# Kernel optimization log

Hardware: AMD Instinct MI355X
Metric: run time of the kernel (lower is better)

## Reference

```python
import jax, jax.numpy as jnp
import numpy as np

N = 8192
HID = 256
LAMBDA = 1.0
MU = 1.0
DIM = 2
GC = 0.0027
L = 0.02
Y0, Y1 = 0.0, 1.0
STRESS_PRE_SCALE = 1.0
PF_PRE_SCALE = 1.0


def loading(t):
    # linear displacement loading
    return t[0]


def mlp(Ws, bs, inp):
    h = inp
    for W, b in zip(Ws[:-1], bs[:-1]):
        h = jnp.tanh(h @ W + b)
    return h @ Ws[-1] + bs[-1]


def net_u(Ws, bs, x, t):
    sol = mlp(Ws, bs, jnp.concatenate([x, t]))  # (3,)
    phi = jax.nn.sigmoid(sol[:1])               # (1,)
    ld = loading(t)
    ux = (x[1] - Y0) * (x[1] - Y1) * sol[1:2] * ld / 3.0
    uy = (x[1] - Y0) * (x[1] - Y1) * sol[2:3] * ld + (x[1] - Y0) / (Y1 - Y0) * ld
    return phi, jnp.concatenate([ux, uy])       # (1,), (2,)


def epsilon_fn(Ws, bs, x, t):
    J = jax.jacrev(lambda xx: net_u(Ws, bs, xx, t)[1])(x)  # (2,2)
    return (J + J.T) / 2.0


def psi_pos(eps):
    tr = jnp.trace(eps)
    k = LAMBDA + MU * 2.0 / DIM
    dev = eps - tr * jnp.eye(DIM, dtype=eps.dtype) / DIM
    return k * jax.nn.relu(tr) ** 2 / 2 + MU * jnp.trace(dev @ dev)


def psi_neg(eps):
    k = LAMBDA + MU * 2.0 / DIM
    return k * jax.nn.relu(-jnp.trace(eps)) ** 2 / 2


def sigma_fn(Ws, bs, x, t):
    phi, _ = net_u(Ws, bs, x, t)
    g_phi = (1 - phi[0]) ** 2 + 1e-6
    eps = epsilon_fn(Ws, bs, x, t)
    return g_phi * jax.grad(psi_pos)(eps) + jax.grad(psi_neg)(eps)


def net_stress(Ws, bs, x, t):
    def damaged(xx):
        phi, _ = net_u(Ws, bs, xx, t)
        return (1 - phi) ** 2 * sigma_fn(Ws, bs, xx, t)  # (2,2)
    D = jax.jacrev(damaged)(x)          # (2,2,2)
    return jnp.einsum('ijj->i', D) / STRESS_PRE_SCALE


def net_pf_raw(Ws, bs, x, t):
    phi, _ = net_u(Ws, bs, x, t)
    phi0 = phi[0]
    eps = epsilon_fn(Ws, bs, x, t)
    H = jax.hessian(lambda xx: net_u(Ws, bs, xx, t)[0])(x)[0]  # (2,2)
    lap_phi = jnp.trace(H)
    pf = GC * (phi0 / L - L * lap_phi) - 2 * (1 - phi0) * psi_pos(eps)
    return pf / PF_PRE_SCALE


def net_speed(Ws, bs, x, t):
    return jax.jacrev(lambda tt: net_u(Ws, bs, x, tt)[0])(t)[0, 0]


def net_pf(Ws, bs, x, t):
    pf = net_pf_raw(Ws, bs, x, t)
    dphi_dt = net_speed(Ws, bs, x, t)
    phi0 = net_u(Ws, bs, x, t)[0][0]
    mask_pos = (jnp.abs(dphi_dt) <= 1e-3) & (jnp.abs(phi0 - 1) > 1e-3)
    mask_neg = jnp.abs(phi0 - 1) <= 1e-3
    return jnp.where(mask_pos, jax.nn.relu(-pf), jnp.where(mask_neg, jax.nn.relu(pf), pf))


def net_energy(Ws, bs, x, t):
    phi0 = net_u(Ws, bs, x, t)[0][0]
    eps = epsilon_fn(Ws, bs, x, t)
    nphi = jax.jacrev(lambda xx: net_u(Ws, bs, xx, t)[0])(x)[0]  # (2,)
    return ((1 - phi0) * 2 * psi_pos(eps) + psi_neg(eps)
            + GC * (phi0 ** 2 / (2 * L) + L / 2 * jnp.sum(nphi ** 2)))


def _forward(W0, W1, W2, W3, W4, b0, b1, b2, b3, b4, x, t):
    Ws = [W0, W1, W2, W3, W4]
    bs = [b0, b1, b2, b3, b4]
    res_s = jax.vmap(net_stress, in_axes=(None, None, 0, 0))(Ws, bs, x, t)   # (N,2)
    res_pf = jax.vmap(net_pf, in_axes=(None, None, 0, 0))(Ws, bs, x, t)     # (N,)
    res_e = jax.vmap(net_energy, in_axes=(None, None, 0, 0))(Ws, bs, x, t)  # (N,)
    dphi = jax.vmap(net_speed, in_axes=(None, None, 0, 0))(Ws, bs, x, t)    # (N,)
    # component re-weighting for the vector stress residual (as in loss_pde)
    mse_res = jnp.mean(res_s ** 2, axis=0)  # (2,)
    w = jax.lax.stop_gradient(jnp.mean(mse_res) / (mse_res + 1e-6))
    r = jnp.sqrt(jnp.sum(res_s ** 2 * w[None, :], axis=-1))
    loss_stress = jnp.mean(r ** 2)
    loss_pf = jnp.mean(res_pf ** 2)
    loss_energy = jnp.log(jnp.sum(res_e))
    loss_irr = jnp.mean(jax.nn.relu(-dphi))
    return jnp.stack([loss_stress, loss_pf, loss_energy, loss_irr])


def setup_inputs() -> dict:
    key = jax.random.key(0)
    dims = [3, HID, HID, HID, HID, 3]
    ks = jax.random.split(key, 12)
    inp = {}
    for i in range(5):
        fan_in, fan_out = dims[i], dims[i + 1]
        inp[f'W{i}'] = (jax.random.normal(ks[i], (fan_in, fan_out), jnp.float32)
                        * np.sqrt(2.0 / (fan_in + fan_out)).astype(np.float32))
        inp[f'b{i}'] = jnp.zeros((fan_out,), jnp.float32)
    inp['x'] = jax.random.uniform(ks[10], (N, 2), jnp.float32, 0.0, 1.0)
    inp['t'] = jax.random.uniform(ks[11], (N, 1), jnp.float32, 0.05, 1.0)
    return inp


def reference(W0, W1, W2, W3, W4, b0, b1, b2, b3, b4, x, t):
    return _forward(W0, W1, W2, W3, W4, b0, b1, b2, b3, b4, x, t)
```

## Files before the change

### kernel.cpp

```cpp
#include <hip/hip_runtime.h>
#include <math.h>

#define N_PTS 8192
#define HIDDEN 256
#define PPB 8
#define THREADS 256
#define NBLK (N_PTS / PPB)
#define NBINS 64
#define LDA 264
#define AROWS 62
#define LDZ 264
#define BP_OFF 4096

typedef float f32x4 __attribute__((ext_vector_type(4)));
typedef short s8v  __attribute__((ext_vector_type(8)));
typedef short s4v  __attribute__((ext_vector_type(4)));

__device__ __forceinline__ unsigned short bf16_rne(float x) {
    unsigned int u = __float_as_uint(x);
    return (unsigned short)((u + 0x7FFFu + ((u >> 16) & 1u)) >> 16);
}
__device__ __forceinline__ float bf16f(unsigned short h) {
    return __uint_as_float(((unsigned int)h) << 16);
}
__device__ __forceinline__ int rowof(int s, int p) {
    return (s < 6) ? ((s >> 1) * 16 + (p >> 1) * 4 + (p & 1) * 2 + (s & 1))
                   : (48 + (p >> 1) * 4 + (p & 1));
}

__global__ void pinn_pack(const float* __restrict__ W1, const float* __restrict__ W2,
                          const float* __restrict__ W3, unsigned short* __restrict__ Bp,
                          float* __restrict__ bins)
{
    if (blockIdx.x == 0) {
        bins[threadIdx.x] = 0.f;
        bins[threadIdx.x + 256] = 0.f;
        if (threadIdx.x == 0) *(unsigned*)(bins + 512) = 0u;
    }
    const int id = blockIdx.x * 256 + threadIdx.x;
    const int lane = id & 63;
    const int nt   = (id >> 6) & 15;
    const int kc   = (id >> 10) & 7;
    const int l    = id >> 13;
    const float* W = (l == 0) ? W1 : ((l == 1) ? W2 : W3);
    const int n  = nt * 16 + (lane & 15);
    unsigned short hi[8], lo[8];
    #pragma unroll
    for (int i = 0; i < 8; ++i) {
        const int kslot = kc * 32 + (lane >> 4) * 8 + i;
        const int korig = ((kslot >> 6) & 3) * 64 + (kslot & 3) * 16 + ((kslot >> 2) & 15);
        const float x = W[(size_t)korig * HIDDEN + n];
        const unsigned short h = bf16_rne(x);
        hi[i] = h;
        lo[i] = bf16_rne(x - bf16f(h));
    }
    const size_t bh = ((((size_t)(l * 2 + 0) * 8 + kc) * 16 + nt) * 64 + lane) * 8;
    const size_t bl = ((((size_t)(l * 2 + 1) * 8 + kc) * 16 + nt) * 64 + lane) * 8;
    *(s8v*)&Bp[bh] = *(const s8v*)hi;
    *(s8v*)&Bp[bl] = *(const s8v*)lo;
}

__global__ __launch_bounds__(THREADS, 2)
void pinn_main(const float* __restrict__ W0, const float* __restrict__ b0,
               const float* __restrict__ b1, const float* __restrict__ b2,
               const float* __restrict__ b3,
               const float* __restrict__ W4, const float* __restrict__ b4,
               const float* __restrict__ xin, const float* __restrict__ tin,
               const unsigned short* __restrict__ Bp,
               float* __restrict__ bins, float* __restrict__ out)
{
    __shared__ __align__(16) unsigned char LB[65472];
    short* __restrict__ AhS = (short*)LB;
    short* __restrict__ AlS = (short*)(LB + AROWS * LDA * 2);
    float* __restrict__ Zf  = (float*)LB;

    const int tid  = threadIdx.x;
    const int lane = tid & 63;
    const int w    = tid >> 6;
    const int c    = lane & 15;
    const int g    = lane >> 4;
    const int pt0  = blockIdx.x * PPB;
    unsigned* cnt  = (unsigned*)(bins + 512);

    {
        const int c0i = tid & 15, w0i = (tid >> 4) & 3, pp = tid >> 6;
        float w0v[4], w1v[4], w2v[4], bbv[4];
        #pragma unroll
        for (int nn = 0; nn < 4; ++nn) {
            const int j = w0i * 64 + 16 * nn + c0i;
            w0v[nn] = W0[j]; w1v[nn] = W0[HIDDEN + j]; w2v[nn] = W0[2 * HIDDEN + j];
            bbv[nn] = b0[j];
        }
        const int sbase = 4 * (c0i + 16 * w0i);
        #pragma unroll
        for (int e = 0; e < 2; ++e) {
            const int p = pp + 4 * e;
            const float x0 = xin[(pt0 + p) * 2 + 0];
            const float x1 = xin[(pt0 + p) * 2 + 1];
            const float tt = tin[pt0 + p];
            s4v hi[7], lo[7];
            #pragma unroll
            for (int nn = 0; nn < 4; ++nn) {
                const float z  = fmaf(x0, w0v[nn], fmaf(x1, w1v[nn], fmaf(tt, w2v[nn], bbv[nn])));
                const float a  = tanhf(z);
                const float st = 1.f - a * a;
                const float m2 = -2.f * a * st;
                float v[7];
                v[0] = a;
                v[1] = st * w0v[nn]; v[2] = st * w1v[nn]; v[3] = st * w2v[nn];
                v[4] = m2 * w0v[nn] * w0v[nn];
                v[5] = m2 * w0v[nn] * w1v[nn];
                v[6] = m2 * w1v[nn] * w1v[nn];
                #pragma unroll
                for (int s = 0; s < 7; ++s) {
                    const unsigned short h = bf16_rne(v[s]);
                    hi[s][nn] = (short)h;
                    lo[s][nn] = (short)bf16_rne(v[s] - bf16f(h));
                }
            }
            #pragma unroll
            for (int s = 0; s < 7; ++s) {
                const int r = rowof(s, p);
                *(s4v*)&AhS[r * LDA + sbase] = hi[s];
                *(s4v*)&AlS[r * LDA + sbase] = lo[s];
            }
        }
        if (pp == 0) {
            const s4v z4 = {0, 0, 0, 0};
            #pragma unroll
            for (int b = 0; b < 3; ++b)
                #pragma unroll
                for (int d = 2; d < 4; ++d) {
                    const int r = 48 + 4 * b + d;
                    *(s4v*)&AhS[r * LDA + sbase] = z4;
                    *(s4v*)&AlS[r * LDA + sbase] = z4;
                }
        }
    }
    __syncthreads();

    int aoff[4];
    #pragma unroll
    for (int mt = 0; mt < 3; ++mt) aoff[mt] = (16 * mt + c) * LDA + g * 8;
    aoff[3] = (48 + ((c >= 14) ? 0 : c)) * LDA + g * 8;

    for (int l = 0; l < 3; ++l) {
        f32x4 acc[4][4];
        #pragma unroll
        for (int mt = 0; mt < 4; ++mt)
            #pragma unroll
            for (int nn = 0; nn < 4; ++nn) acc[mt][nn] = (f32x4)0.f;

        const size_t lbase = (size_t)l * 2 * 8 * 16 * 64 * 8;
        #pragma unroll
        for (int kc = 0; kc < 8; ++kc) {
            s8v ah[4], al[4];
            #pragma unroll
            for (int mt = 0; mt < 4; ++mt) {
                ah[mt] = *(const s8v*)&AhS[aoff[mt] + kc * 32];
                al[mt] = *(const s8v*)&AlS[aoff[mt] + kc * 32];
            }
            s8v bh[4], bl[4];
            #pragma unroll
            for (int nn = 0; nn < 4; ++nn) {
                const int nt = w * 4 + nn;
                const size_t oh = lbase + (((size_t)kc * 16 + nt) * 64 + lane) * 8;
                const size_t ol = oh + (size_t)8 * 16 * 64 * 8;
                bh[nn] = *(const s8v*)&Bp[oh];
                bl[nn] = *(const s8v*)&Bp[ol];
            }
            #pragma unroll
            for (int mt = 0; mt < 4; ++mt)
                #pragma unroll
                for (int nn = 0; nn < 4; ++nn) {
                    acc[mt][nn] = __builtin_amdgcn_mfma_f32_16x16x32_bf16(ah[mt], bh[nn], acc[mt][nn], 0, 0, 0);
                    acc[mt][nn] = __builtin_amdgcn_mfma_f32_16x16x32_bf16(ah[mt], bl[nn], acc[mt][nn], 0, 0, 0);
                    acc[mt][nn] = __builtin_amdgcn_mfma_f32_16x16x32_bf16(al[mt], bh[nn], acc[mt][nn], 0, 0, 0);
                }
        }
        __syncthreads();

        const float* bias = (l == 0) ? b1 : (l == 1) ? b2 : b3;
        float bbv[4];
        #pragma unroll
        for (int nn = 0; nn < 4; ++nn) bbv[nn] = bias[64 * w + 16 * nn + c];
        const int sbase = 4 * (c + 16 * w);

        #pragma unroll
        for (int e = 0; e < 2; ++e) {
            const int p = 2 * g + e;
            float v[7][4];
            #pragma unroll
            for (int nn = 0; nn < 4; ++nn) {
                const float z0 = acc[0][nn][2 * e + 0] + bbv[nn];
                const float z1 = acc[0][nn][2 * e + 1];
                const float z2 = acc[1][nn][2 * e + 0];
                const float z3 = acc[1][nn][2 * e + 1];
                const float z4 = acc[2][nn][2 * e + 0];
                const float z5 = acc[2][nn][2 * e + 1];
                const float z6 = acc[3][nn][e];
                const float a  = tanhf(z0);
                const float st = 1.f - a * a;
                const float m2 = -2.f * a * st;
                v[0][nn] = a;
                v[1][nn] = st * z1; v[2][nn] = st * z2; v[3][nn] = st * z3;
                v[4][nn] = fmaf(m2 * z1, z1, st * z4);
                v[5][nn] = fmaf(m2 * z1, z2, st * z5);
                v[6][nn] = fmaf(m2 * z2, z2, st * z6);
            }
            if (l < 2) {
                #pragma unroll
                for (int s = 0; s < 7; ++s) {
                    s4v hi, lo;
                    #pragma unroll
                    for (int nn = 0; nn < 4; ++nn) {
                        const unsigned short h = bf16_rne(v[s][nn]);
                        hi[nn] = (short)h;
                        lo[nn] = (short)bf16_rne(v[s][nn] - bf16f(h));
                    }
                    const int r = rowof(s, p);
                    *(s4v*)&AhS[r * LDA + sbase] = hi;
                    *(s4v*)&AlS[r * LDA + sbase] = lo;
                }
            } else {
                #pragma unroll
                for (int s = 0; s < 7; ++s) {
                    f32x4 vv = {v[s][0], v[s][1], v[s][2], v[s][3]};
                    *(f32x4*)&Zf[(8 * s + p) * LDZ + sbase] = vv;
                }
            }
        }
        __syncthreads();
    }

    const int h  = (lane >> 5);
    const int la = lane & 31;
    const int p  = w * 2 + h;

    float part[7][3];
    #pragma unroll
    for (int s = 0; s < 7; ++s)
        #pragma unroll
        for (int m = 0; m < 3; ++m) part[s][m] = 0.f;

    #pragma unroll
    for (int i = 0; i < 8; ++i) {
        const int kslot = la + 32 * i;
        const int korig = ((kslot >> 6) & 3) * 64 + (kslot & 3) * 16 + ((kslot >> 2) & 15);
        const float w40 = W4[korig * 3 + 0], w41 = W4[korig * 3 + 1], w42 = W4[korig * 3 + 2];
        #pragma unroll
        for (int s = 0; s < 7; ++s) {
            const float hk = Zf[(8 * s + p) * LDZ + kslot];
            part[s][0] = fmaf(hk, w40, part[s][0]);
            part[s][1] = fmaf(hk, w41, part[s][1]);
            part[s][2] = fmaf(hk, w42, part[s][2]);
        }
    }
    #pragma unroll
    for (int s = 0; s < 7; ++s)
        #pragma unroll
        for (int m = 0; m < 3; ++m) {
            float v = part[s][m];
            #pragma unroll
            for (int off = 16; off > 0; off >>= 1) v += __shfl_xor(v, off);
            part[s][m] = v;
        }

    const float x0 = xin[(pt0 + p) * 2 + 0];
    const float x1 = xin[(pt0 + p) * 2 + 1];
    const float tt = tin[pt0 + p];

    const float V0 = part[0][0] + b4[0];
    const float V1 = part[0][1] + b4[1];
    const float V2 = part[0][2] + b4[2];
    const float J00 = part[1][0], J01 = part[2][0], J0t = part[3][0];
    const float J10 = part[1][1], J11 = part[2][1];
    const float J20 = part[1][2], J21 = part[2][2];
    const float H000 = part[4][0], H011 = part[6][0];
    const float H100 = part[4][1], H101 = part[5][1], H111 = part[6][1];
    const float H200 = part[4][2], H201 = part[5][2], H211 = part[6][2];

    const float phi = 1.f / (1.f + expf(-V0));
    const float om  = 1.f - phi;
    const float sp  = phi * om;
    const float spp = sp * (1.f - 2.f * phi);
    const float phx0 = sp * J00, phx1 = sp * J01, dphidt = sp * J0t;
    const float lap = spp * (J00 * J00 + J01 * J01) + sp * (H000 + H011);

    const float ld = tt;
    const float qq = x1 * (x1 - 1.f), qp = 2.f * x1 - 1.f;

    const float ux0 = qq * J10 * ld * (1.f / 3.f);
    const float ux1 = (qp * V1 + qq * J11) * ld * (1.f / 3.f);
    const float uy0 = qq * J20 * ld;
    const float uy1 = (qp * V2 + qq * J21) * ld + ld;

    const float e00 = ux0, e11 = uy1, e01 = 0.5f * (ux1 + uy0);
    const float tr = e00 + e11;

    const float ux_00 = qq * H100 * ld * (1.f / 3.f);
    const float ux_01 = (qp * J10 + qq * H101) * ld * (1.f / 3.f);
    const float ux_11 = (2.f * V1 + 2.f * qp * J11 + qq * H111) * ld * (1.f / 3.f);
    const float uy_00 = qq * H200 * ld;
    const float uy_01 = (qp * J20 + qq * H201) * ld;
    const float uy_11 = (2.f * V2 + 2.f * qp * J21 + qq * H211) * ld;

    const float de00_0 = ux_00, de00_1 = ux_01;
    const float de11_0 = uy_01, de11_1 = uy_11;
    const float de01_0 = 0.5f * (ux_01 + uy_00), de01_1 = 0.5f * (ux_11 + uy_01);
    const float dtr_0 = de00_0 + de11_0, dtr_1 = de00_1 + de11_1;

    const float kk = 2.f;
    const float rtr = fmaxf(tr, 0.f), rntr = fmaxf(-tr, 0.f);
    const float Hp = (tr > 0.f) ? 1.f : 0.f, Hn = (tr < 0.f) ? 1.f : 0.f;

    const float dv = 0.5f * (e00 - e11);
    const float sp00 = kk * rtr + 2.f * dv;
    const float sp11 = kk * rtr - 2.f * dv;
    const float sp01 = 2.f * e01;
    const float snd  = -kk * rntr;

    const float dsp00_0 = kk * Hp * dtr_0 + 2.f * (de00_0 - 0.5f * dtr_0);
    const float dsp01_0 = 2.f * de01_0;
    const float dsp01_1 = 2.f * de01_1;
    const float dsp11_1 = kk * Hp * dtr_1 + 2.f * (de11_1 - 0.5f * dtr_1);
    const float dsn_0 = kk * Hn * dtr_0, dsn_1 = kk * Hn * dtr_1;

    const float cc  = om * om, gg = cc + 1e-6f;
    const float dc0 = -2.f * om * phx0, dc1 = -2.f * om * phx1;
    const float gpc = gg + cc, cg = cc * gg;

    const float res0 = dc0 * gpc * sp00 + cg * dsp00_0 + dc0 * snd + cc * dsn_0
                     + dc1 * gpc * sp01 + cg * dsp01_1;
    const float res1 = dc0 * gpc * sp01 + cg * dsp01_0
                     + dc1 * gpc * sp11 + cg * dsp11_1 + dc1 * snd + cc * dsn_1;

    const float psip = rtr * rtr + 0.5f * (e00 - e11) * (e00 - e11) + 2.f * e01 * e01;
    const float psin = rntr * rntr;

    const float GCc = 0.0027f, LL = 0.02f;
    const float pf = GCc * (phi / LL - LL * lap) - 2.f * om * psip;
    const bool maskp = (fabsf(dphidt) <= 1e-3f) && (fabsf(phi - 1.f) > 1e-3f);
    const bool maskn = fabsf(phi - 1.f) <= 1e-3f;
    const float respf = maskp ? fmaxf(-pf, 0.f) : (maskn ? fmaxf(pf, 0.f) : pf);

    const float rese = om * 2.f * psip + psin
                     + GCc * (phi * phi / (2.f * LL)
                              + 0.5f * LL * (phx0 * phx0 + phx1 * phx1));
    const float irr = fmaxf(-dphidt, 0.f);

    if (la == 0) {
        float* bin = bins + (blockIdx.x & (NBINS - 1)) * 8;
        atomicAdd(bin + 0, res0 * res0);
        atomicAdd(bin + 1, res1 * res1);
        atomicAdd(bin + 2, respf * respf);
        atomicAdd(bin + 3, rese);
        atomicAdd(bin + 4, irr);
    }

    __syncthreads();
    volatile unsigned* flg = (volatile unsigned*)(LB + 65024);
    if (tid == 0) {
        const unsigned old = atomicAdd(cnt, 1u);
        *flg = old;
    }
    __syncthreads();
    if (*flg == NBLK - 1) {
        if (tid < 64) {
            float s0 = atomicAdd(&bins[tid * 8 + 0], 0.f);
            float s1 = atomicAdd(&bins[tid * 8 + 1], 0.f);
            float s2 = atomicAdd(&bins[tid * 8 + 2], 0.f);
            float s3 = atomicAdd(&bins[tid * 8 + 3], 0.f);
            float s4 = atomicAdd(&bins[tid * 8 + 4], 0.f);
            #pragma unroll
            for (int off = 32; off > 0; off >>= 1) {
                s0 += __shfl_xor(s0, off);
                s1 += __shfl_xor(s1, off);
                s2 += __shfl_xor(s2, off);
                s3 += __shfl_xor(s3, off);
                s4 += __shfl_xor(s4, off);
            }
            if (tid == 0) {
                const float inv_n = 1.f / (float)N_PTS;
                const float mse0 = s0 * inv_n, mse1 = s1 * inv_n;
                const float wm = 0.5f * (mse0 + mse1);
                out[0] = wm * mse0 / (mse0 + 1e-6f) + wm * mse1 / (mse1 + 1e-6f);
                out[1] = s2 * inv_n;
                out[2] = logf(s3);
                out[3] = s4 * inv_n;
            }
        }
    }
}

extern "C" void kernel_launch(void* const* d_in, const int* in_sizes, int n_in,
                              void* d_out, int out_size, void* d_ws, size_t ws_size,
                              hipStream_t stream)
{
    const float *W[5], *b[5];
    if (in_sizes[1] == HIDDEN) {
        for (int i = 0; i < 5; ++i) {
            W[i] = (const float*)d_in[2 * i];
            b[i] = (const float*)d_in[2 * i + 1];
        }
    } else {
        for (int i = 0; i < 5; ++i) {
            W[i] = (const float*)d_in[i];
            b[i] = (const float*)d_in[5 + i];
        }
    }
    const float* x = (const float*)d_in[10];
    const float* t = (const float*)d_in[11];
    float* bins = (float*)d_ws;
    unsigned short* Bp = (unsigned short*)((char*)d_ws + BP_OFF);

    pinn_pack<<<96, 256, 0, stream>>>(W[1], W[2], W[3], Bp, bins);
    pinn_main<<<NBLK, THREADS, 0, stream>>>(W[0], b[0], b[1], b[2], b[3],
                                            W[4], b[4], x, t, Bp, bins,
                                            (float*)d_out);
}
```

Before: 155.1 us.

## Halve points per block and repack A rows to remove MFMA padding waste

```diff
diff --git a/kernel.cpp b/kernel.cpp
--- a/kernel.cpp
+++ b/kernel.cpp
@@ -3,12 +3,12 @@
 
 #define N_PTS 8192
 #define HIDDEN 256
-#define PPB 8
+#define PPB 4
 #define THREADS 256
 #define NBLK (N_PTS / PPB)
 #define NBINS 64
 #define LDA 264
-#define AROWS 62
+#define AROWS 32
 #define LDZ 264
 #define BP_OFF 4096
 
@@ -24,20 +24,15 @@
     return __uint_as_float(((unsigned int)h) << 16);
 }
 __device__ __forceinline__ int rowof(int s, int p) {
-    return (s < 6) ? ((s >> 1) * 16 + (p >> 1) * 4 + (p & 1) * 2 + (s & 1))
-                   : (48 + (p >> 1) * 4 + (p & 1));
+    return (s < 4) ? (4 * p + s) : (16 + 4 * p + (s - 4));
 }
 
 __global__ void pinn_pack(const float* __restrict__ W1, const float* __restrict__ W2,
                           const float* __restrict__ W3, unsigned short* __restrict__ Bp,
                           float* __restrict__ bins)
 {
-    if (blockIdx.x == 0) {
-        bins[threadIdx.x] = 0.f;
-        bins[threadIdx.x + 256] = 0.f;
-        if (threadIdx.x == 0) *(unsigned*)(bins + 512) = 0u;
-    }
-    const int id = blockIdx.x * 256 + threadIdx.x;
+    const int id = blockIdx.x * 64 + threadIdx.x;
+    if (id < 520) bins[id] = 0.f;
     const int lane = id & 63;
     const int nt   = (id >> 6) & 15;
     const int kc   = (id >> 10) & 7;
@@ -60,7 +55,7 @@
     *(s8v*)&Bp[bl] = *(const s8v*)lo;
 }
 
-__global__ __launch_bounds__(THREADS, 2)
+__global__ __launch_bounds__(THREADS, 4)
 void pinn_main(const float* __restrict__ W0, const float* __restrict__ b0,
                const float* __restrict__ b1, const float* __restrict__ b2,
                const float* __restrict__ b3,
@@ -69,7 +64,8 @@
                const unsigned short* __restrict__ Bp,
                float* __restrict__ bins, float* __restrict__ out)
 {
-    __shared__ __align__(16) unsigned char LB[65472];
+    __shared__ __align__(16) unsigned char LB[AROWS * LDA * 4];
+    __shared__ unsigned flagS;
     short* __restrict__ AhS = (short*)LB;
     short* __restrict__ AlS = (short*)(LB + AROWS * LDA * 2);
     float* __restrict__ Zf  = (float*)LB;
@@ -92,71 +88,59 @@
             bbv[nn] = b0[j];
         }
         const int sbase = 4 * (c0i + 16 * w0i);
-        #pragma unroll
-        for (int e = 0; e < 2; ++e) {
-            const int p = pp + 4 * e;
-            const float x0 = xin[(pt0 + p) * 2 + 0];
-            const float x1 = xin[(pt0 + p) * 2 + 1];
-            const float tt = tin[pt0 + p];
-            s4v hi[7], lo[7];
-            #pragma unroll
-            for (int nn = 0; nn < 4; ++nn) {
-                const float z  = fmaf(x0, w0v[nn], fmaf(x1, w1v[nn], fmaf(tt, w2v[nn], bbv[nn])));
-                const float a  = tanhf(z);
-                const float st = 1.f - a * a;
-                const float m2 = -2.f * a * st;
-                float v[7];
-                v[0] = a;
-                v[1] = st * w0v[nn]; v[2] = st * w1v[nn]; v[3] = st * w2v[nn];
-                v[4] = m2 * w0v[nn] * w0v[nn];
-                v[5] = m2 * w0v[nn] * w1v[nn];
-                v[6] = m2 * w1v[nn] * w1v[nn];
-                #pragma unroll
-                for (int s = 0; s < 7; ++s) {
-                    const unsigned short h = bf16_rne(v[s]);
-                    hi[s][nn] = (short)h;
-                    lo[s][nn] = (short)bf16_rne(v[s] - bf16f(h));
-                }
-            }
+        const float x0 = xin[(pt0 + pp) * 2 + 0];
+        const float x1 = xin[(pt0 + pp) * 2 + 1];
+        const float tt = tin[pt0 + pp];
+        s4v hi[7], lo[7];
+        #pragma unroll
+        for (int nn = 0; nn < 4; ++nn) {
+            const float z  = fmaf(x0, w0v[nn], fmaf(x1, w1v[nn], fmaf(tt, w2v[nn], bbv[nn])));
+            const float a  = tanhf(z);
+            const float st = 1.f - a * a;
+            const float m2 = -2.f * a * st;
+            float v[7];
+            v[0] = a;
+            v[1] = st * w0v[nn]; v[2] = st * w1v[nn]; v[3] = st * w2v[nn];
+            v[4] = m2 * w0v[nn] * w0v[nn];
+            v[5] = m2 * w0v[nn] * w1v[nn];
+            v[6] = m2 * w1v[nn] * w1v[nn];
             #pragma unroll
             for (int s = 0; s < 7; ++s) {
-                const int r = rowof(s, p);
-                *(s4v*)&AhS[r * LDA + sbase] = hi[s];
-                *(s4v*)&AlS[r * LDA + sbase] = lo[s];
-            }
-        }
-        if (pp == 0) {
-            const s4v z4 = {0, 0, 0, 0};
-            #pragma unroll
-            for (int b = 0; b < 3; ++b)
-                #pragma unroll
-                for (int d = 2; d < 4; ++d) {
-                    const int r = 48 + 4 * b + d;
-                    *(s4v*)&AhS[r * LDA + sbase] = z4;
-                    *(s4v*)&AlS[r * LDA + sbase] = z4;
-                }
-        }
+                const unsigned short h = bf16_rne(v[s]);
+                hi[s][nn] = (short)h;
+                lo[s][nn] = (short)bf16_rne(v[s] - bf16f(h));
+            }
+        }
+        #pragma unroll
+        for (int s = 0; s < 7; ++s) {
+            const int r = rowof(s, pp);
+            *(s4v*)&AhS[r * LDA + sbase] = hi[s];
+            *(s4v*)&AlS[r * LDA + sbase] = lo[s];
+        }
+        const s4v z4 = {0, 0, 0, 0};
+        const int rp = 16 + 4 * pp + 3;
+        *(s4v*)&AhS[rp * LDA + sbase] = z4;
+        *(s4v*)&AlS[rp * LDA + sbase] = z4;
     }
     __syncthreads();
 
-    int aoff[4];
-    #pragma unroll
-    for (int mt = 0; mt < 3; ++mt) aoff[mt] = (16 * mt + c) * LDA + g * 8;
-    aoff[3] = (48 + ((c >= 14) ? 0 : c)) * LDA + g * 8;
+    int aoff[2];
+    #pragma unroll
+    for (int mt = 0; mt < 2; ++mt) aoff[mt] = (16 * mt + c) * LDA + g * 8;
 
     for (int l = 0; l < 3; ++l) {
-        f32x4 acc[4][4];
-        #pragma unroll
-        for (int mt = 0; mt < 4; ++mt)
+        f32x4 acc[2][4];
+        #pragma unroll
+        for (int mt = 0; mt < 2; ++mt)
             #pragma unroll
             for (int nn = 0; nn < 4; ++nn) acc[mt][nn] = (f32x4)0.f;
 
         const size_t lbase = (size_t)l * 2 * 8 * 16 * 64 * 8;
         #pragma unroll
         for (int kc = 0; kc < 8; ++kc) {
-            s8v ah[4], al[4];
-            #pragma unroll
-            for (int mt = 0; mt < 4; ++mt) {
+            s8v ah[2], al[2];
+            #pragma unroll
+            for (int mt = 0; mt < 2; ++mt) {
                 ah[mt] = *(const s8v*)&AhS[aoff[mt] + kc * 32];
                 al[mt] = *(const s8v*)&AlS[aoff[mt] + kc * 32];
             }
@@ -170,7 +154,7 @@
                 bl[nn] = *(const s8v*)&Bp[ol];
             }
             #pragma unroll
-            for (int mt = 0; mt < 4; ++mt)
+            for (int mt = 0; mt < 2; ++mt)
                 #pragma unroll
                 for (int nn = 0; nn < 4; ++nn) {
                     acc[mt][nn] = __builtin_amdgcn_mfma_f32_16x16x32_bf16(ah[mt], bh[nn], acc[mt][nn], 0, 0, 0);
@@ -186,57 +170,50 @@
         for (int nn = 0; nn < 4; ++nn) bbv[nn] = bias[64 * w + 16 * nn + c];
         const int sbase = 4 * (c + 16 * w);
 
-        #pragma unroll
-        for (int e = 0; e < 2; ++e) {
-            const int p = 2 * g + e;
-            float v[7][4];
-            #pragma unroll
-            for (int nn = 0; nn < 4; ++nn) {
-                const float z0 = acc[0][nn][2 * e + 0] + bbv[nn];
-                const float z1 = acc[0][nn][2 * e + 1];
-                const float z2 = acc[1][nn][2 * e + 0];
-                const float z3 = acc[1][nn][2 * e + 1];
-                const float z4 = acc[2][nn][2 * e + 0];
-                const float z5 = acc[2][nn][2 * e + 1];
-                const float z6 = acc[3][nn][e];
-                const float a  = tanhf(z0);
-                const float st = 1.f - a * a;
-                const float m2 = -2.f * a * st;
-                v[0][nn] = a;
-                v[1][nn] = st * z1; v[2][nn] = st * z2; v[3][nn] = st * z3;
-                v[4][nn] = fmaf(m2 * z1, z1, st * z4);
-                v[5][nn] = fmaf(m2 * z1, z2, st * z5);
-                v[6][nn] = fmaf(m2 * z2, z2, st * z6);
-            }
-            if (l < 2) {
+        float v[7][4];
+        #pragma unroll
+        for (int nn = 0; nn < 4; ++nn) {
+            const float z0 = acc[0][nn][0] + bbv[nn];
+            const float z1 = acc[0][nn][1];
+            const float z2 = acc[0][nn][2];
+            const float z3 = acc[0][nn][3];
+            const float z4 = acc[1][nn][0];
+            const float z5 = acc[1][nn][1];
+            const float z6 = acc[1][nn][2];
+            const float a  = tanhf(z0);
+            const float st = 1.f - a * a;
+            const float m2 = -2.f * a * st;
+            v[0][nn] = a;
+            v[1][nn] = st * z1; v[2][nn] = st * z2; v[3][nn] = st * z3;
+            v[4][nn] = fmaf(m2 * z1, z1, st * z4);
+            v[5][nn] = fmaf(m2 * z1, z2, st * z5);
+            v[6][nn] = fmaf(m2 * z2, z2, st * z6);
+        }
+        if (l < 2) {
+            #pragma unroll
+            for (int s = 0; s < 7; ++s) {
+                s4v hi, lo;
                 #pragma unroll
-                for (int s = 0; s < 7; ++s) {
-                    s4v hi, lo;
-                    #pragma unroll
-                    for (int nn = 0; nn < 4; ++nn) {
-                        const unsigned short h = bf16_rne(v[s][nn]);
-                        hi[nn] = (short)h;
-                        lo[nn] = (short)bf16_rne(v[s][nn] - bf16f(h));
-                    }
-                    const int r = rowof(s, p);
-                    *(s4v*)&AhS[r * LDA + sbase] = hi;
-                    *(s4v*)&AlS[r * LDA + sbase] = lo;
+                for (int nn = 0; nn < 4; ++nn) {
+                    const unsigned short h = bf16_rne(v[s][nn]);
+                    hi[nn] = (short)h;
+                    lo[nn] = (short)bf16_rne(v[s][nn] - bf16f(h));
                 }
-            } else {
-                #pragma unroll
-                for (int s = 0; s < 7; ++s) {
-                    f32x4 vv = {v[s][0], v[s][1], v[s][2], v[s][3]};
-                    *(f32x4*)&Zf[(8 * s + p) * LDZ + sbase] = vv;
-                }
+                const int r = rowof(s, g);
+                *(s4v*)&AhS[r * LDA + sbase] = hi;
+                *(s4v*)&AlS[r * LDA + sbase] = lo;
+            }
+        } else {
+            #pragma unroll
+            for (int s = 0; s < 7; ++s) {
+                f32x4 vv = {v[s][0], v[s][1], v[s][2], v[s][3]};
+                *(f32x4*)&Zf[rowof(s, g) * LDZ + sbase] = vv;
             }
         }
         __syncthreads();
     }
 
-    const int h  = (lane >> 5);
-    const int la = lane & 31;
-    const int p  = w * 2 + h;
-
+    const int p = w;
     float part[7][3];
     #pragma unroll
     for (int s = 0; s < 7; ++s)
@@ -244,13 +221,13 @@
         for (int m = 0; m < 3; ++m) part[s][m] = 0.f;
 
     #pragma unroll
-    for (int i = 0; i < 8; ++i) {
-        const int kslot = la + 32 * i;
+    for (int i = 0; i < 4; ++i) {
+        const int kslot = lane + 64 * i;
         const int korig = ((kslot >> 6) & 3) * 64 + (kslot & 3) * 16 + ((kslot >> 2) & 15);
         const float w40 = W4[korig * 3 + 0], w41 = W4[korig * 3 + 1], w42 = W4[korig * 3 + 2];
         #pragma unroll
         for (int s = 0; s < 7; ++s) {
-            const float hk = Zf[(8 * s + p) * LDZ + kslot];
+            const float hk = Zf[rowof(s, p) * LDZ + kslot];
             part[s][0] = fmaf(hk, w40, part[s][0]);
             part[s][1] = fmaf(hk, w41, part[s][1]);
             part[s][2] = fmaf(hk, w42, part[s][2]);
@@ -262,7 +239,7 @@
         for (int m = 0; m < 3; ++m) {
             float v = part[s][m];
             #pragma unroll
-            for (int off = 16; off > 0; off >>= 1) v += __shfl_xor(v, off);
+            for (int off = 32; off > 0; off >>= 1) v += __shfl_xor(v, off);
             part[s][m] = v;
         }
 
@@ -349,7 +326,7 @@
                               + 0.5f * LL * (phx0 * phx0 + phx1 * phx1));
     const float irr = fmaxf(-dphidt, 0.f);
 
-    if (la == 0) {
+    if (lane == 0) {
         float* bin = bins + (blockIdx.x & (NBINS - 1)) * 8;
         atomicAdd(bin + 0, res0 * res0);
         atomicAdd(bin + 1, res1 * res1);
@@ -359,36 +336,30 @@
     }
 
     __syncthreads();
-    volatile unsigned* flg = (volatile unsigned*)(LB + 65024);
-    if (tid == 0) {
-        const unsigned old = atomicAdd(cnt, 1u);
-        *flg = old;
-    }
+    if (tid == 0) flagS = atomicAdd(cnt, 1u);
     __syncthreads();
-    if (*flg == NBLK - 1) {
-        if (tid < 64) {
-            float s0 = atomicAdd(&bins[tid * 8 + 0], 0.f);
-            float s1 = atomicAdd(&bins[tid * 8 + 1], 0.f);
-            float s2 = atomicAdd(&bins[tid * 8 + 2], 0.f);
-            float s3 = atomicAdd(&bins[tid * 8 + 3], 0.f);
-            float s4 = atomicAdd(&bins[tid * 8 + 4], 0.f);
-            #pragma unroll
-            for (int off = 32; off > 0; off >>= 1) {
-                s0 += __shfl_xor(s0, off);
-                s1 += __shfl_xor(s1, off);
-                s2 += __shfl_xor(s2, off);
-                s3 += __shfl_xor(s3, off);
-                s4 += __shfl_xor(s4, off);
-            }
-            if (tid == 0) {
-                const float inv_n = 1.f / (float)N_PTS;
-                const float mse0 = s0 * inv_n, mse1 = s1 * inv_n;
-                const float wm = 0.5f * (mse0 + mse1);
-                out[0] = wm * mse0 / (mse0 + 1e-6f) + wm * mse1 / (mse1 + 1e-6f);
-                out[1] = s2 * inv_n;
-                out[2] = logf(s3);
-                out[3] = s4 * inv_n;
-            }
+    if (flagS == NBLK - 1 && tid < 64) {
+        float s0 = atomicAdd(&bins[tid * 8 + 0], 0.f);
+        float s1 = atomicAdd(&bins[tid * 8 + 1], 0.f);
+        float s2 = atomicAdd(&bins[tid * 8 + 2], 0.f);
+        float s3 = atomicAdd(&bins[tid * 8 + 3], 0.f);
+        float s4 = atomicAdd(&bins[tid * 8 + 4], 0.f);
+        #pragma unroll
+        for (int off = 32; off > 0; off >>= 1) {
+            s0 += __shfl_xor(s0, off);
+            s1 += __shfl_xor(s1, off);
+            s2 += __shfl_xor(s2, off);
+            s3 += __shfl_xor(s3, off);
+            s4 += __shfl_xor(s4, off);
+        }
+        if (tid == 0) {
+            const float inv_n = 1.f / (float)N_PTS;
+            const float mse0 = s0 * inv_n, mse1 = s1 * inv_n;
+            const float wm = 0.5f * (mse0 + mse1);
+            out[0] = wm * mse0 / (mse0 + 1e-6f) + wm * mse1 / (mse1 + 1e-6f);
+            out[1] = s2 * inv_n;
+            out[2] = logf(s3);
+            out[3] = s4 * inv_n;
         }
     }
 }
@@ -414,7 +385,7 @@
     float* bins = (float*)d_ws;
     unsigned short* Bp = (unsigned short*)((char*)d_ws + BP_OFF);
 
-    pinn_pack<<<96, 256, 0, stream>>>(W[1], W[2], W[3], Bp, bins);
+    pinn_pack<<<384, 64, 0, stream>>>(W[1], W[2], W[3], Bp, bins);
     pinn_main<<<NBLK, THREADS, 0, stream>>>(W[0], b[0], b[1], b[2], b[3],
                                             W[4], b[4], x, t, Bp, bins,
                                             (float*)d_out);
```

Result: slower. 179.2 us (+15.5%).
